# Kernel optimization log

Hardware: AMD Instinct MI355X
Metric: run time of the kernel (lower is better)

The kernel has to match this reference:

```python
import jax, jax.numpy as jnp
import numpy as np
from jax import lax


def setup_inputs() -> dict:
    key = jax.random.key(0)
    k0, k1, k2, k3 = jax.random.split(key, 4)
    B, C, H, W = 16, 64, 192, 192
    K = 3
    x0 = jax.random.normal(k0, (B, C, H, W), dtype=jnp.float32)
    d = jax.random.normal(k1, (B, C), dtype=jnp.float32)
    w1 = jax.random.normal(k2, (C, C), dtype=jnp.float32) * 0.05
    w2 = jax.random.normal(k3, (C * K * K, C), dtype=jnp.float32) * 0.05
    return {"x0": x0, "d": d, "w1": w1, "w2": w2}


def reference(x0, d, w1, w2):
    b, c, h, w = x0.shape
    k = int(round((w2.shape[0] // c) ** 0.5))  # kernel_size
    # kernel-generating MLP: Linear(C,C,bias=False) -> LeakyReLU(0.1) -> Linear(C,C*k*k,bias=False)
    hid = jax.nn.leaky_relu(d @ w1.T, negative_slope=0.1)          # (B, C)
    ker = (hid @ w2.T).reshape(b * c, 1, k, k)                      # (B*C, 1, k, k)
    pad = (k - 1) // 2
    # per-(batch,channel) dynamic depthwise conv: groups = B*C
    out = lax.conv_general_dilated(
        x0.reshape(1, b * c, h, w),
        ker,
        window_strides=(1, 1),
        padding=[(pad, pad), (pad, pad)],
        dimension_numbers=("NCHW", "OIHW", "NCHW"),
        feature_group_count=b * c,
    )
    return out.reshape(b, c, h, w)
```

## Files before the change

kernel.cpp:

```cpp
#include <hip/hip_runtime.h>


#define BB 16
#define CC 64
#define HH 192
#define WW 192
#define KK2 9
#define KERLEN (CC * KK2)

__global__ __launch_bounds__(256) void gen_kernels(
    const float* __restrict__ d,
    const float* __restrict__ w1,
    const float* __restrict__ w2,
    float* __restrict__ ker)
{
    __shared__ float dd[CC];
    __shared__ float hid[CC];
    const int b = blockIdx.x;
    const int t = threadIdx.x;

    if (t < CC) dd[t] = d[b * CC + t];
    __syncthreads();

    if (t < CC) {
        const float* w1r = w1 + t * CC;
        float acc = 0.f;
        #pragma unroll 8
        for (int m = 0; m < CC; ++m) acc += dd[m] * w1r[m];
        hid[t] = acc > 0.f ? acc : 0.1f * acc;
    }
    __syncthreads();

    for (int o = t; o < KERLEN; o += 256) {
        const float* w2r = w2 + o * CC;
        float acc = 0.f;
        #pragma unroll 8
        for (int k = 0; k < CC; ++k) acc += hid[k] * w2r[k];
        ker[b * KERLEN + o] = acc;
    }
}

__global__ __launch_bounds__(256) void dconv3x3(
    const float* __restrict__ x,
    const float* __restrict__ ker,
    float* __restrict__ out)
{
    const int QW = WW / 4;
    const int bc = blockIdx.x;
    const float* __restrict__ xp = x + (size_t)bc * HH * WW;
    float* __restrict__ op = out + (size_t)bc * HH * WW;

    const float* kp = ker + bc * KK2;
    float kk[9];
    #pragma unroll
    for (int i = 0; i < 9; ++i) kk[i] = kp[i];

    for (int idx = threadIdx.x; idx < HH * QW; idx += 256) {
        const int h = idx / QW;
        const int qw = idx - h * QW;
        const int w = qw * 4;

        float a0 = 0.f, a1 = 0.f, a2 = 0.f, a3 = 0.f;
        #pragma unroll
        for (int dh = -1; dh <= 1; ++dh) {
            const int r = h + dh;
            if (r < 0 || r >= HH) continue;
            const float* row = xp + r * WW + w;
            const float4 c = *(const float4*)row;
            const float v0 = (w > 0) ? row[-1] : 0.f;
            const float v5 = (w + 4 < WW) ? row[4] : 0.f;
            const float v1 = c.x, v2 = c.y, v3 = c.z, v4 = c.w;
            const float k0 = kk[(dh + 1) * 3 + 0];
            const float k1 = kk[(dh + 1) * 3 + 1];
            const float k2 = kk[(dh + 1) * 3 + 2];
            a0 += k0 * v0 + k1 * v1 + k2 * v2;
            a1 += k0 * v1 + k1 * v2 + k2 * v3;
            a2 += k0 * v2 + k1 * v3 + k2 * v4;
            a3 += k0 * v3 + k1 * v4 + k2 * v5;
        }
        *(float4*)(op + h * WW + w) = make_float4(a0, a1, a2, a3);
    }
}

extern "C" void kernel_launch(void* const* d_in, const int* in_sizes, int n_in,
                              void* d_out, int out_size, void* d_ws, size_t ws_size,
                              hipStream_t stream) {
    const float* x0 = (const float*)d_in[0];
    const float* d  = (const float*)d_in[1];
    const float* w1 = (const float*)d_in[2];
    const float* w2 = (const float*)d_in[3];
    float* out = (float*)d_out;
    float* ker = (float*)d_ws;

    gen_kernels<<<BB, 256, 0, stream>>>(d, w1, w2, ker);
    dconv3x3<<<BB * CC, 256, 0, stream>>>(x0, ker, out);
}
```

Measured before the change: 306.8 us.

## Fuse kernel generation into depthwise conv and split each plane across four blocks

Merges the MLP kernel-generation kernel into the convolution kernel, so each block recomputes the hidden vector and its own nine taps instead of reading them from a workspace written by a separate launch. The grid also grows fourfold, with each block handling a quarter of the rows of one plane, to raise parallelism. This removes one launch and the serialization between the two kernels. In exchange, each block redundantly performs the 64x64 first-layer matvec, which adds latency at the start of every block.

```diff
diff --git a/kernel.cpp b/kernel.cpp
--- a/kernel.cpp
+++ b/kernel.cpp
@@ -5,19 +5,27 @@
 #define CC 64
 #define HH 192
 #define WW 192
-#define KK2 9
-#define KERLEN (CC * KK2)
+#define SPLIT 4
+#define ROWS (HH / SPLIT)
+#define QW (WW / 4)
 
-__global__ __launch_bounds__(256) void gen_kernels(
+__global__ __launch_bounds__(256) void fused_ddc(
+    const float* __restrict__ x,
     const float* __restrict__ d,
     const float* __restrict__ w1,
     const float* __restrict__ w2,
-    float* __restrict__ ker)
+    float* __restrict__ out)
 {
     __shared__ float dd[CC];
     __shared__ float hid[CC];
-    const int b = blockIdx.x;
-    const int t = threadIdx.x;
+    __shared__ float kks[9];
+
+    const int blk   = blockIdx.x;
+    const int bc    = blk >> 2;
+    const int slice = blk & 3;
+    const int b     = bc >> 6;
+    const int c     = bc & 63;
+    const int t     = threadIdx.x;
 
     if (t < CC) dd[t] = d[b * CC + t];
     __syncthreads();
@@ -31,34 +39,31 @@
     }
     __syncthreads();
 
-    for (int o = t; o < KERLEN; o += 256) {
-        const float* w2r = w2 + o * CC;
-        float acc = 0.f;
+    if (t < 9) {
+        const float* w2r = w2 + (c * 9 + t) * CC;
+        float a0 = 0.f, a1 = 0.f;
         #pragma unroll 8
-        for (int k = 0; k < CC; ++k) acc += hid[k] * w2r[k];
-        ker[b * KERLEN + o] = acc;
+        for (int k = 0; k < CC; k += 2) {
+            a0 += hid[k]     * w2r[k];
+            a1 += hid[k + 1] * w2r[k + 1];
+        }
+        kks[t] = a0 + a1;
     }
-}
+    __syncthreads();
 
-__global__ __launch_bounds__(256) void dconv3x3(
-    const float* __restrict__ x,
-    const float* __restrict__ ker,
-    float* __restrict__ out)
-{
-    const int QW = WW / 4;
-    const int bc = blockIdx.x;
-    const float* __restrict__ xp = x + (size_t)bc * HH * WW;
-    float* __restrict__ op = out + (size_t)bc * HH * WW;
-
-    const float* kp = ker + bc * KK2;
     float kk[9];
     #pragma unroll
-    for (int i = 0; i < 9; ++i) kk[i] = kp[i];
+    for (int i = 0; i < 9; ++i) kk[i] = kks[i];
 
-    for (int idx = threadIdx.x; idx < HH * QW; idx += 256) {
-        const int h = idx / QW;
-        const int qw = idx - h * QW;
-        const int w = qw * 4;
+    const float* __restrict__ xp = x   + (size_t)bc * HH * WW;
+    float* __restrict__       op = out + (size_t)bc * HH * WW;
+    const int h0 = slice * ROWS;
+
+    for (int idx = t; idx < ROWS * QW; idx += 256) {
+        const int hl = idx / QW;
+        const int qw = idx - hl * QW;
+        const int h  = h0 + hl;
+        const int w  = qw * 4;
 
         float a0 = 0.f, a1 = 0.f, a2 = 0.f, a3 = 0.f;
         #pragma unroll
@@ -66,17 +71,16 @@
             const int r = h + dh;
             if (r < 0 || r >= HH) continue;
             const float* row = xp + r * WW + w;
-            const float4 c = *(const float4*)row;
-            const float v0 = (w > 0) ? row[-1] : 0.f;
-            const float v5 = (w + 4 < WW) ? row[4] : 0.f;
-            const float v1 = c.x, v2 = c.y, v3 = c.z, v4 = c.w;
+            const float4 cv = *(const float4*)row;
+            const float v0 = (w > 0)       ? row[-1] : 0.f;
+            const float v5 = (w + 4 < WW)  ? row[4]  : 0.f;
             const float k0 = kk[(dh + 1) * 3 + 0];
             const float k1 = kk[(dh + 1) * 3 + 1];
             const float k2 = kk[(dh + 1) * 3 + 2];
-            a0 += k0 * v0 + k1 * v1 + k2 * v2;
-            a1 += k0 * v1 + k1 * v2 + k2 * v3;
-            a2 += k0 * v2 + k1 * v3 + k2 * v4;
-            a3 += k0 * v3 + k1 * v4 + k2 * v5;
+            a0 += k0 * v0   + k1 * cv.x + k2 * cv.y;
+            a1 += k0 * cv.x + k1 * cv.y + k2 * cv.z;
+            a2 += k0 * cv.y + k1 * cv.z + k2 * cv.w;
+            a3 += k0 * cv.z + k1 * cv.w + k2 * v5;
         }
         *(float4*)(op + h * WW + w) = make_float4(a0, a1, a2, a3);
     }
@@ -90,8 +94,6 @@
     const float* w1 = (const float*)d_in[2];
     const float* w2 = (const float*)d_in[3];
     float* out = (float*)d_out;
-    float* ker = (float*)d_ws;
 
-    gen_kernels<<<BB, 256, 0, stream>>>(d, w1, w2, ker);
-    dconv3x3<<<BB * CC, 256, 0, stream>>>(x0, ker, out);
+    fused_ddc<<<BB * CC * SPLIT, 256, 0, stream>>>(x0, d, w1, w2, out);
 }
```

Result: no change. 305.3 us (-0.5%).

## Slide a 3-row register window per thread over row strips in depthwise conv

Applied to the files above, without the earlier changes.

Each thread now handles a 4-wide column over 12 consecutive rows and keeps the previous two rows in registers, so each input row is loaded once instead of three times. The grid is split into 3 blocks per (batch,channel) plane for more parallelism, and boundary handling uses clamped loads with selects instead of branches. Outputs are written with nontemporal stores to avoid cache pollution. This costs more registers per thread and fewer independent threads per plane.

```diff
diff --git a/kernel.cpp b/kernel.cpp
--- a/kernel.cpp
+++ b/kernel.cpp
@@ -5,8 +5,13 @@
 #define CC 64
 #define HH 192
 #define WW 192
-#define KK2 9
-#define KERLEN (CC * KK2)
+#define KERLEN (CC * 9)
+#define QW (WW / 4)
+#define RPT 12
+#define TPP (QW * (HH / RPT))
+#define BPP (TPP / 256)
+
+typedef float f4 __attribute__((ext_vector_type(4)));
 
 __global__ __launch_bounds__(256) void gen_kernels(
     const float* __restrict__ d,
@@ -40,45 +45,75 @@
     }
 }
 
-__global__ __launch_bounds__(256) void dconv3x3(
+__global__ __launch_bounds__(256, 4) void dconv3x3_v3(
     const float* __restrict__ x,
     const float* __restrict__ ker,
     float* __restrict__ out)
 {
-    const int QW = WW / 4;
-    const int bc = blockIdx.x;
-    const float* __restrict__ xp = x + (size_t)bc * HH * WW;
-    float* __restrict__ op = out + (size_t)bc * HH * WW;
+    const int blk = blockIdx.x;
+    const int bc  = blk / BPP;
+    const int sub = blk - bc * BPP;
 
-    const float* kp = ker + bc * KK2;
-    float kk[9];
+    const float* kp = ker + bc * 9;
+    const float k00 = kp[0], k01 = kp[1], k02 = kp[2];
+    const float k10 = kp[3], k11 = kp[4], k12 = kp[5];
+    const float k20 = kp[6], k21 = kp[7], k22 = kp[8];
+
+    const int task = sub * 256 + threadIdx.x;
+    const int rg   = task / QW;
+    const int qw   = task - rg * QW;
+    const int w    = qw * 4;
+    const int r0   = rg * RPT;
+
+    const bool hasL = (qw > 0);
+    const bool hasR = (qw < QW - 1);
+    const int  offL = hasL ? -1 : 0;
+    const int  offR = hasR ?  4 : 0;
+
+    const float* __restrict__ xp = x   + (size_t)bc * HH * WW + w;
+    float* __restrict__       op = out + (size_t)bc * HH * WW + w;
+
+    f4 ca, cb, cc;
+    float la, lb, lc, ra, rb, rc;
+    const f4 zero = {0.f, 0.f, 0.f, 0.f};
+
+    auto ld = [&](int rr, f4& c, float& l, float& r) {
+        const int rcl = rr < 0 ? 0 : (rr >= HH ? HH - 1 : rr);
+        const float* p = xp + rcl * WW;
+        const f4 v     = *(const f4*)p;
+        const float lv = p[offL];
+        const float rv = p[offR];
+        const bool ok  = (rr >= 0) & (rr < HH);
+        c = ok ? v : zero;
+        l = (ok && hasL) ? lv : 0.f;
+        r = (ok && hasR) ? rv : 0.f;
+    };
+
+    ld(r0 - 1, ca, la, ra);
+    ld(r0,     cb, lb, rb);
+
     #pragma unroll
-    for (int i = 0; i < 9; ++i) kk[i] = kp[i];
+    for (int i = 0; i < RPT; ++i) {
+        ld(r0 + i + 1, cc, lc, rc);
 
-    for (int idx = threadIdx.x; idx < HH * QW; idx += 256) {
-        const int h = idx / QW;
-        const int qw = idx - h * QW;
-        const int w = qw * 4;
+        f4 o;
+        o.x = k00 * la   + k01 * ca.x + k02 * ca.y
+            + k10 * lb   + k11 * cb.x + k12 * cb.y
+            + k20 * lc   + k21 * cc.x + k22 * cc.y;
+        o.y = k00 * ca.x + k01 * ca.y + k02 * ca.z
+            + k10 * cb.x + k11 * cb.y + k12 * cb.z
+            + k20 * cc.x + k21 * cc.y + k22 * cc.z;
+        o.z = k00 * ca.y + k01 * ca.z + k02 * ca.w
+            + k10 * cb.y + k11 * cb.z + k12 * cb.w
+            + k20 * cc.y + k21 * cc.z + k22 * cc.w;
+        o.w = k00 * ca.z + k01 * ca.w + k02 * ra
+            + k10 * cb.z + k11 * cb.w + k12 * rb
+            + k20 * cc.z + k21 * cc.w + k22 * rc;
 
-        float a0 = 0.f, a1 = 0.f, a2 = 0.f, a3 = 0.f;
-        #pragma unroll
-        for (int dh = -1; dh <= 1; ++dh) {
-            const int r = h + dh;
-            if (r < 0 || r >= HH) continue;
-            const float* row = xp + r * WW + w;
-            const float4 c = *(const float4*)row;
-            const float v0 = (w > 0) ? row[-1] : 0.f;
-            const float v5 = (w + 4 < WW) ? row[4] : 0.f;
-            const float v1 = c.x, v2 = c.y, v3 = c.z, v4 = c.w;
-            const float k0 = kk[(dh + 1) * 3 + 0];
-            const float k1 = kk[(dh + 1) * 3 + 1];
-            const float k2 = kk[(dh + 1) * 3 + 2];
-            a0 += k0 * v0 + k1 * v1 + k2 * v2;
-            a1 += k0 * v1 + k1 * v2 + k2 * v3;
-            a2 += k0 * v2 + k1 * v3 + k2 * v4;
-            a3 += k0 * v3 + k1 * v4 + k2 * v5;
-        }
-        *(float4*)(op + h * WW + w) = make_float4(a0, a1, a2, a3);
+        __builtin_nontemporal_store(o, (f4*)(op + (size_t)(r0 + i) * WW));
+
+        ca = cb; la = lb; ra = rb;
+        cb = cc; lb = lc; rb = rc;
     }
 }
 
@@ -93,5 +128,5 @@
     float* ker = (float*)d_ws;
 
     gen_kernels<<<BB, 256, 0, stream>>>(d, w1, w2, ker);
-    dconv3x3<<<BB * CC, 256, 0, stream>>>(x0, ker, out);
+    dconv3x3_v3<<<BB * CC * BPP, 256, 0, stream>>>(x0, ker, out);
 }
```

After: 275.0 us. -10.4%, faster.
